# Kernel optimization log

Hardware: AMD Instinct MI355X
Metric: run time of the kernel (lower is better)

The kernel has to match this reference:

```python
import jax, jax.numpy as jnp
import numpy as np

B, S, HID = 4, 2048, 1024
NH, NKV, HD = 16, 4, 64
GROUPS = NH // NKV
SCALE = HD ** -0.5


def make_rope(seq_len, dim, base=10000.0):
    inv_freq = 1.0 / (base ** (np.arange(0, dim, 2, dtype=np.float32) / dim))
    t = np.arange(seq_len, dtype=np.float32)
    freqs = np.outer(t, inv_freq)                      # [S, D/2]
    emb = np.concatenate([freqs, freqs], axis=-1)      # [S, D] duplicated-half convention
    cos = jnp.asarray(np.cos(emb))[None, None]         # [1,1,S,D]
    sin = jnp.asarray(np.sin(emb))[None, None]
    return cos, sin


def setup_inputs() -> dict:
    key = jax.random.key(0)
    ks = jax.random.split(key, 8)
    hidden_states = jax.random.normal(ks[0], (B, S, HID), dtype=jnp.float32)
    cos, sin = make_rope(S, HD)
    std = HID ** -0.5
    Wq = jax.random.normal(ks[1], (NH * HD, HID), dtype=jnp.float32) * std
    bq = jnp.zeros((NH * HD,), dtype=jnp.float32)
    Wk = jax.random.normal(ks[2], (NKV * HD, HID), dtype=jnp.float32) * std
    bk = jnp.zeros((NKV * HD,), dtype=jnp.float32)
    Wv = jax.random.normal(ks[3], (NKV * HD, HID), dtype=jnp.float32) * std
    bv = jnp.zeros((NKV * HD,), dtype=jnp.float32)
    Wo = jax.random.normal(ks[4], (HID, NH * HD), dtype=jnp.float32) * std
    bo = jnp.zeros((HID,), dtype=jnp.float32)
    return dict(hidden_states=hidden_states, cos=cos, sin=sin,
                Wq=Wq, bq=bq, Wk=Wk, bk=bk, Wv=Wv, bv=bv, Wo=Wo, bo=bo)


def rotate_half(x):
    x1, x2 = jnp.split(x, 2, axis=-1)
    return jnp.concatenate([-x2, x1], axis=-1)


def reference(hidden_states, cos, sin, Wq, bq, Wk, bk, Wv, bv, Wo, bo):
    x = hidden_states  # [B,S,HID]
    q = (x @ Wq.T + bq).reshape(B, S, NH, HD).transpose(0, 2, 1, 3)    # [B,NH,S,D]
    k = (x @ Wk.T + bk).reshape(B, S, NKV, HD).transpose(0, 2, 1, 3)   # [B,NKV,S,D]
    v = (x @ Wv.T + bv).reshape(B, S, NKV, HD).transpose(0, 2, 1, 3)
    # RoPE
    q = q * cos + rotate_half(q) * sin
    k = k * cos + rotate_half(k) * sin
    # GQA: repeat_interleave kv heads to match q heads
    k = jnp.repeat(k, GROUPS, axis=1)  # [B,NH,S,D]
    v = jnp.repeat(v, GROUPS, axis=1)
    # scaled dot-product attention (no mask, no dropout at eval)
    scores = jnp.einsum('bhqd,bhkd->bhqk', q, k) * SCALE
    attn = jax.nn.softmax(scores, axis=-1)
    out = jnp.einsum('bhqk,bhkd->bhqd', attn, v)       # [B,NH,S,D]
    out = out.transpose(0, 2, 1, 3).reshape(B, S, NH * HD)
    return out @ Wo.T + bo
```

## Files before the change

### kernel.cpp

```cpp
#include <hip/hip_runtime.h>
#include <stdint.h>

#define S_LEN 2048
#define HIDDEN 1024
#define NHEADS 16
#define NKVH 4
#define HDIM 64

typedef __bf16 bf16x8 __attribute__((ext_vector_type(8)));
typedef __bf16 bf16x4 __attribute__((ext_vector_type(4)));
typedef float f32x4 __attribute__((ext_vector_type(4)));
typedef short s16x4 __attribute__((ext_vector_type(4)));
typedef unsigned short U16;

#define OFF_XB   0u
#define OFF_WQB  8388608u
#define OFF_WKB  9437184u
#define OFF_WVB  9699328u
#define OFF_WOB  9961472u
#define OFF_Q    11010048u
#define OFF_K    19398656u
#define OFF_V    21495808u
#define OFF_AWS  OFF_XB

static __device__ __forceinline__ U16 f2bf(float f){
    unsigned u;
    __builtin_memcpy(&u, &f, 4);
    u += 0x7FFFu + ((u >> 16) & 1u);
    return (U16)(u >> 16);
}
static __device__ __forceinline__ uint32_t pkbf(float lo, float hi){
    uint32_t a, b;
    __builtin_memcpy(&a, &lo, 4); a += 0x7FFFu + ((a >> 16) & 1u);
    __builtin_memcpy(&b, &hi, 4); b += 0x7FFFu + ((b >> 16) & 1u);
    return (a >> 16) | (b & 0xFFFF0000u);
}

typedef __attribute__((address_space(3))) uint32_t lds_u32;
typedef const __attribute__((address_space(1))) uint32_t glb_u32;
static __device__ __forceinline__ void glds16(const U16* g, U16* l){
    __builtin_amdgcn_global_load_lds((glb_u32*)g, (lds_u32*)l, 16, 0, 0);
}

__global__ void conv_kernel(const float* __restrict__ X,  const float* __restrict__ Wq,
                            const float* __restrict__ Wk, const float* __restrict__ Wv,
                            const float* __restrict__ Wo, U16* __restrict__ dst)
{
    size_t i4 = (size_t)blockIdx.x * 256 + threadIdx.x;
    size_t e = i4 * 4;
    const float* s;
    if (e < 8388608u)       s = X  + e;
    else if (e < 9437184u)  s = Wq + (e - 8388608u);
    else if (e < 9699328u)  s = Wk + (e - 9437184u);
    else if (e < 9961472u)  s = Wv + (e - 9699328u);
    else                    s = Wo + (e - 9961472u);
    float4 v = *(const float4*)s;
    uint2 o; o.x = pkbf(v.x, v.y); o.y = pkbf(v.z, v.w);
    *(uint2*)(dst + e) = o;
}

__global__ __launch_bounds__(256, 3)
void qkv_kernel(const U16* __restrict__ Xb,
                const U16* __restrict__ Wqb, const U16* __restrict__ Wkb, const U16* __restrict__ Wvb,
                const float* __restrict__ bq, const float* __restrict__ bk, const float* __restrict__ bv,
                const float* __restrict__ cosT, const float* __restrict__ sinT,
                U16* __restrict__ qws, U16* __restrict__ kws, U16* __restrict__ vtws)
{
    __shared__ __align__(16) U16 Asm[128 * 64];
    __shared__ __align__(16) U16 Bsm[128 * 64];

    const int mblk = blockIdx.x;
    const int nblk = blockIdx.y;
    const int tid  = threadIdx.x;
    const int wave = tid >> 6, lane = tid & 63;
    const int ln = lane & 15, quad = lane >> 4;
    const int wm = wave >> 1, wn = wave & 1;

    const U16* Wp; const float* biasp; int region;
    const int nbase = nblk * 128;
    if (nblk < 8)       { Wp = Wqb + (size_t)nbase * HIDDEN;          biasp = bq + nbase;          region = 0; }
    else if (nblk < 10) { Wp = Wkb + (size_t)(nbase - 1024) * HIDDEN; biasp = bk + (nbase - 1024); region = 1; }
    else                { Wp = Wvb + (size_t)(nbase - 1280) * HIDDEN; biasp = bv + (nbase - 1280); region = 2; }
    const U16* Xp = Xb + (size_t)mblk * 128 * HIDDEN;

    f32x4 acc[4][4];
    #pragma unroll
    for (int i = 0; i < 4; i++)
        #pragma unroll
        for (int j = 0; j < 4; j++) acc[i][j] = (f32x4){0.f, 0.f, 0.f, 0.f};

    const int l8 = lane >> 3;
    const int cg = (lane & 7) ^ l8;
    const int sw = ln & 7;

    for (int k0 = 0; k0 < HIDDEN; k0 += 64) {
        __syncthreads();
        #pragma unroll
        for (int t = 0; t < 4; t++) {
            int rbase = wave * 32 + t * 8;
            glds16(Xp + (size_t)(rbase + l8) * HIDDEN + k0 + cg * 8, &Asm[rbase * 64]);
            glds16(Wp + (size_t)(rbase + l8) * HIDDEN + k0 + cg * 8, &Bsm[rbase * 64]);
        }
        __syncthreads();

        bf16x8 af[4][2], bfr[4][2];
        #pragma unroll
        for (int i = 0; i < 4; i++)
            #pragma unroll
            for (int ks = 0; ks < 2; ks++) {
                af[i][ks]  = *(const bf16x8*)(&Asm[(wm * 64 + i * 16 + ln) * 64 + (((ks * 4 + quad) ^ sw) * 8)]);
                bfr[i][ks] = *(const bf16x8*)(&Bsm[(wn * 64 + i * 16 + ln) * 64 + (((ks * 4 + quad) ^ sw) * 8)]);
            }
        #pragma unroll
        for (int i = 0; i < 4; i++)
            #pragma unroll
            for (int j = 0; j < 4; j++) {
                acc[i][j] = __builtin_amdgcn_mfma_f32_16x16x32_bf16(af[i][0], bfr[j][0], acc[i][j], 0, 0, 0);
                acc[i][j] = __builtin_amdgcn_mfma_f32_16x16x32_bf16(af[i][1], bfr[j][1], acc[i][j], 0, 0, 0);
            }
    }

    float bias[4];
    #pragma unroll
    for (int j = 0; j < 4; j++) bias[j] = biasp[wn * 64 + j * 16 + ln];

    const float QSCALE = 0.125f * 1.44269504089f;

    if (region == 2) {
        #pragma unroll
        for (int i = 0; i < 4; i++) {
            int m0 = mblk * 128 + wm * 64 + i * 16 + quad * 4;
            int b = m0 >> 11;
            int st6 = m0 & (S_LEN - 1);
            int tile = st6 >> 6, soff = st6 & 63;
            #pragma unroll
            for (int j = 0; j < 4; j++) {
                int n2 = nbase - 1280 + wn * 64 + j * 16 + ln;
                int hh = n2 >> 6, d = n2 & 63;
                uint2 w;
                w.x = pkbf(acc[i][j][0] + bias[j], acc[i][j][1] + bias[j]);
                w.y = pkbf(acc[i][j][2] + bias[j], acc[i][j][3] + bias[j]);
                *(uint2*)(vtws + ((((size_t)b * NKVH + hh) * 32 + tile) * 64 + d) * 64 + soff) = w;
            }
        }
    } else {
        #pragma unroll
        for (int i = 0; i < 4; i++) {
            #pragma unroll
            for (int r = 0; r < 4; r++) {
                int m = mblk * 128 + wm * 64 + i * 16 + quad * 4 + r;
                int s = m & (S_LEN - 1), b = m >> 11;
                float vals[4];
                #pragma unroll
                for (int j = 0; j < 4; j++) vals[j] = acc[i][j][r] + bias[j];
                float outv[4];
                #pragma unroll
                for (int j = 0; j < 4; j++) {
                    int d = (wn * 64 + j * 16 + ln) & 63;
                    float c  = cosT[s * HDIM + d];
                    float sn = sinT[s * HDIM + d];
                    float partner = vals[j ^ 2];
                    float rot = (d < 32) ? -partner : partner;
                    outv[j] = vals[j] * c + rot * sn;
                }
                if (region == 0) {
                    #pragma unroll
                    for (int j = 0; j < 4; j++) {
                        int n = nbase + wn * 64 + j * 16 + ln;
                        int hh = n >> 6, d = n & 63;
                        qws[(((size_t)b * NHEADS + hh) * S_LEN + s) * HDIM + d] = f2bf(outv[j] * QSCALE);
                    }
                } else {
                    #pragma unroll
                    for (int j = 0; j < 4; j++) {
                        int n2 = nbase - 1024 + wn * 64 + j * 16 + ln;
                        int hh = n2 >> 6, d = n2 & 63;
                        kws[(((size_t)b * NKVH + hh) * S_LEN + s) * HDIM + d] = f2bf(outv[j]);
                    }
                }
            }
        }
    }
}

__global__ __launch_bounds__(256, 2)
void attn_kernel(const U16* __restrict__ qws, const U16* __restrict__ kws,
                 const U16* __restrict__ vtws, U16* __restrict__ aws)
{
    __shared__ __align__(16) U16 Ksm[2][64 * 64];
    __shared__ __align__(16) U16 VTsm[2][64 * 64];

    const int qt = blockIdx.x;
    const int hg = blockIdx.y;
    const int b = hg >> 4, h = hg & 15, hkv = h >> 2;
    const U16* Qh  = qws  + (size_t)hg * S_LEN * HDIM;
    const U16* Kh  = kws  + (size_t)(b * NKVH + hkv) * S_LEN * HDIM;
    const U16* VTh = vtws + (size_t)(b * NKVH + hkv) * HDIM * S_LEN;

    const int tid = threadIdx.x;
    const int wave = tid >> 6, lane = tid & 63;
    const int ln = lane & 15, quad = lane >> 4;
    const int sw = ln & 7;
    const int off = (quad & 1) * 4;

    bf16x8 qf[2][2];
    #pragma unroll
    for (int i = 0; i < 2; i++)
        #pragma unroll
        for (int ks = 0; ks < 2; ks++) {
            int row = qt * 128 + wave * 32 + i * 16 + ln;
            qf[i][ks] = *(const bf16x8*)(Qh + (size_t)row * HDIM + ks * 32 + quad * 8);
        }

    float rsA[2] = {0.f, 0.f}, rsB[2] = {0.f, 0.f};
    f32x4 o_t[4][2];
    #pragma unroll
    for (int n = 0; n < 4; n++)
        #pragma unroll
        for (int i = 0; i < 2; i++) o_t[n][i] = (f32x4){0.f, 0.f, 0.f, 0.f};

    const int l8 = lane >> 3;
    const int cgk = (lane & 7) ^ l8;

    const U16* pk[2]; const U16* pv[2];
    U16* dK[2]; U16* dV[2];
    #pragma unroll
    for (int t = 0; t < 2; t++) {
        int c = wave * 2 + t;
        pk[t] = Kh  + (size_t)(c * 8 + l8) * HDIM + cgk * 8;
        pv[t] = VTh + (size_t)(c * 8 + l8) * 64  + cgk * 8;
        dK[t] = &Ksm[0][c * 8 * 64];
        dV[t] = &VTsm[0][c * 8 * 64];
    }

    #pragma unroll
    for (int t = 0; t < 2; t++) {
        glds16(pk[t], dK[t]);
        glds16(pv[t], dV[t]);
        pk[t] += 4096; pv[t] += 4096;
    }

    int p = 0;
    for (int kt = 0; kt < 32; kt++) {
        __syncthreads();

        if (kt < 31) {
            #pragma unroll
            for (int t = 0; t < 2; t++) {
                glds16(pk[t], dK[t] + (p ^ 1) * 4096);
                glds16(pv[t], dV[t] + (p ^ 1) * 4096);
                pk[t] += 4096; pv[t] += 4096;
            }
        }

        bf16x8 kf[4][2];
        #pragma unroll
        for (int j4 = 0; j4 < 4; j4++) {
            int row = j4 * 16 + ln;
            kf[j4][0] = *(const bf16x8*)(&Ksm[p][row * 64 + ((quad ^ sw) * 8)]);
            kf[j4][1] = *(const bf16x8*)(&Ksm[p][row * 64 + (((quad + 4) ^ sw) * 8)]);
        }
        s16x4 vf[4][4];
        #pragma unroll
        for (int j4 = 0; j4 < 4; j4++) {
            int cbase = j4 * 2 + (quad >> 1);
            #pragma unroll
            for (int n = 0; n < 4; n++)
                vf[j4][n] = *(const s16x4*)(&VTsm[p][(n * 16 + ln) * 64 + ((cbase ^ sw) * 8) + off]);
        }
        __builtin_amdgcn_sched_barrier(0);

        #pragma unroll
        for (int j4 = 0; j4 < 4; j4++) {
            s16x4 pf[2];
            #pragma unroll
            for (int i = 0; i < 2; i++) {
                f32x4 z = (f32x4){0.f, 0.f, 0.f, 0.f};
                z = __builtin_amdgcn_mfma_f32_16x16x32_bf16(kf[j4][0], qf[i][0], z, 0, 0, 0);
                z = __builtin_amdgcn_mfma_f32_16x16x32_bf16(kf[j4][1], qf[i][1], z, 0, 0, 0);
                bf16x4 pb;
                #pragma unroll
                for (int r = 0; r < 4; r++) {
                    float pv2 = __builtin_amdgcn_exp2f(z[r]);
                    if (r & 1) rsB[i] += pv2; else rsA[i] += pv2;
                    pb[r] = (__bf16)pv2;
                }
                __builtin_memcpy(&pf[i], &pb, 8);
            }
            #pragma unroll
            for (int n = 0; n < 4; n++) {
                #pragma unroll
                for (int i = 0; i < 2; i++)
                    o_t[n][i] = __builtin_amdgcn_mfma_f32_16x16x16bf16_1k(vf[j4][n], pf[i], o_t[n][i], 0, 0, 0);
            }
        }
        p ^= 1;
    }

    float inv_li[2];
    #pragma unroll
    for (int i = 0; i < 2; i++) {
        float t = rsA[i] + rsB[i];
        t += __shfl_xor(t, 16);
        t += __shfl_xor(t, 32);
        inv_li[i] = 1.f / t;
    }
    #pragma unroll
    for (int n = 0; n < 4; n++)
        #pragma unroll
        for (int i = 0; i < 2; i++) {
            int q = qt * 128 + wave * 32 + i * 16 + ln;
            int d = n * 16 + quad * 4;
            uint2 w;
            w.x = pkbf(o_t[n][i][0] * inv_li[i], o_t[n][i][1] * inv_li[i]);
            w.y = pkbf(o_t[n][i][2] * inv_li[i], o_t[n][i][3] * inv_li[i]);
            *(uint2*)(aws + ((size_t)b * S_LEN + q) * (NHEADS * HDIM) + h * HDIM + d) = w;
        }
}

__global__ __launch_bounds__(256, 3)
void proj_kernel(const U16* __restrict__ A, const U16* __restrict__ Wob,
                 const float* __restrict__ bo, float* __restrict__ out)
{
    __shared__ __align__(16) U16 Asm[128 * 64];
    __shared__ __align__(16) U16 Bsm[128 * 64];

    const int mblk = blockIdx.x;
    const int nblk = blockIdx.y;
    const int tid  = threadIdx.x;
    const int wave = tid >> 6, lane = tid & 63;
    const int ln = lane & 15, quad = lane >> 4;
    const int wm = wave >> 1, wn = wave & 1;

    const int nbase = nblk * 128;
    const U16* Wp = Wob + (size_t)nbase * HIDDEN;
    const U16* Ap = A + (size_t)mblk * 128 * HIDDEN;

    f32x4 acc[4][4];
    #pragma unroll
    for (int i = 0; i < 4; i++)
        #pragma unroll
        for (int j = 0; j < 4; j++) acc[i][j] = (f32x4){0.f, 0.f, 0.f, 0.f};

    const int l8 = lane >> 3;
    const int cg = (lane & 7) ^ l8;
    const int sw = ln & 7;

    for (int k0 = 0; k0 < HIDDEN; k0 += 64) {
        __syncthreads();
        #pragma unroll
        for (int t = 0; t < 4; t++) {
            int rbase = wave * 32 + t * 8;
            glds16(Ap + (size_t)(rbase + l8) * HIDDEN + k0 + cg * 8, &Asm[rbase * 64]);
            glds16(Wp + (size_t)(rbase + l8) * HIDDEN + k0 + cg * 8, &Bsm[rbase * 64]);
        }
        __syncthreads();

        bf16x8 af[4][2], bfr[4][2];
        #pragma unroll
        for (int i = 0; i < 4; i++)
            #pragma unroll
            for (int ks = 0; ks < 2; ks++) {
                af[i][ks]  = *(const bf16x8*)(&Asm[(wm * 64 + i * 16 + ln) * 64 + (((ks * 4 + quad) ^ sw) * 8)]);
                bfr[i][ks] = *(const bf16x8*)(&Bsm[(wn * 64 + i * 16 + ln) * 64 + (((ks * 4 + quad) ^ sw) * 8)]);
            }
        #pragma unroll
        for (int i = 0; i < 4; i++)
            #pragma unroll
            for (int j = 0; j < 4; j++) {
                acc[i][j] = __builtin_amdgcn_mfma_f32_16x16x32_bf16(af[i][0], bfr[j][0], acc[i][j], 0, 0, 0);
                acc[i][j] = __builtin_amdgcn_mfma_f32_16x16x32_bf16(af[i][1], bfr[j][1], acc[i][j], 0, 0, 0);
            }
    }

    float bias[4];
    #pragma unroll
    for (int j = 0; j < 4; j++) bias[j] = bo[nbase + wn * 64 + j * 16 + ln];

    #pragma unroll
    for (int i = 0; i < 4; i++)
        #pragma unroll
        for (int r = 0; r < 4; r++) {
            int m = mblk * 128 + wm * 64 + i * 16 + quad * 4 + r;
            #pragma unroll
            for (int j = 0; j < 4; j++) {
                int n = nbase + wn * 64 + j * 16 + ln;
                out[(size_t)m * HIDDEN + n] = acc[i][j][r] + bias[j];
            }
        }
}

extern "C" void kernel_launch(void* const* d_in, const int* in_sizes, int n_in,
                              void* d_out, int out_size, void* d_ws, size_t ws_size,
                              hipStream_t stream)
{
    const float* X    = (const float*)d_in[0];
    const float* cosT = (const float*)d_in[1];
    const float* sinT = (const float*)d_in[2];
    const float* Wq   = (const float*)d_in[3];
    const float* bq   = (const float*)d_in[4];
    const float* Wk   = (const float*)d_in[5];
    const float* bk   = (const float*)d_in[6];
    const float* Wv   = (const float*)d_in[7];
    const float* bv   = (const float*)d_in[8];
    const float* Wo   = (const float*)d_in[9];
    const float* bo   = (const float*)d_in[10];
    float* out = (float*)d_out;

    U16* wsb = (U16*)d_ws;
    U16* Xb   = wsb + OFF_XB;
    U16* Wqb  = wsb + OFF_WQB;
    U16* Wkb  = wsb + OFF_WKB;
    U16* Wvb  = wsb + OFF_WVB;
    U16* Wob  = wsb + OFF_WOB;
    U16* qws  = wsb + OFF_Q;
    U16* kws  = wsb + OFF_K;
    U16* vtws = wsb + OFF_V;
    U16* aws  = wsb + OFF_AWS;

    conv_kernel<<<dim3(10752), 256, 0, stream>>>(X, Wq, Wk, Wv, Wo, wsb);
    qkv_kernel<<<dim3(64, 12), 256, 0, stream>>>(Xb, Wqb, Wkb, Wvb, bq, bk, bv, cosT, sinT, qws, kws, vtws);
    attn_kernel<<<dim3(16, 64), 256, 0, stream>>>(qws, kws, vtws, aws);
    proj_kernel<<<dim3(64, 8), 256, 0, stream>>>(aws, Wob, bo, out);
}
```

Baseline: 255.3 us.

## Software-pipeline attention inner loop, deferring PV MFMA by one step

Restructures the attention key-tile loop so each step issues the QK^T MFMAs for the current 16-key chunk together with the deferred PV MFMAs from the previous chunk. LDS loads for K and V^T are spread across iterations rather than all issued up front. The chunk's exp2 then runs in the shadow of the matrix work, aiming to hide exp and LDS latency behind MFMA. It also raises launch bounds to 4 blocks per CU and uses s_setprio around the MFMA block. The added carried registers and the tighter register budget from the higher occupancy target could cause spills.

After: 244.7 us. 4.2% less time.

```diff
diff --git a/kernel.cpp b/kernel.cpp
--- a/kernel.cpp
+++ b/kernel.cpp
@@ -183,7 +183,7 @@
     }
 }
 
-__global__ __launch_bounds__(256, 2)
+__global__ __launch_bounds__(256, 4)
 void attn_kernel(const U16* __restrict__ qws, const U16* __restrict__ kws,
                  const U16* __restrict__ vtws, U16* __restrict__ aws)
 {
@@ -201,7 +201,7 @@
     const int wave = tid >> 6, lane = tid & 63;
     const int ln = lane & 15, quad = lane >> 4;
     const int sw = ln & 7;
-    const int off = (quad & 1) * 4;
+    const int voff = (quad & 1) * 4;
 
     bf16x8 qf[2][2];
     #pragma unroll
@@ -221,6 +221,13 @@
 
     const int l8 = lane >> 3;
     const int cgk = (lane & 7) ^ l8;
+
+    const int koff0 = ln * 64 + ((quad ^ sw) * 8);
+    const int koff1 = ln * 64 + (((quad + 4) ^ sw) * 8);
+    const int vbase = ln * 64 + voff;
+    int cvo[4];
+    #pragma unroll
+    for (int j = 0; j < 4; j++) cvo[j] = (((j * 2 + (quad >> 1)) ^ sw) * 8);
 
     const U16* pk[2]; const U16* pv[2];
     U16* dK[2]; U16* dV[2];
@@ -240,6 +247,12 @@
         pk[t] += 4096; pv[t] += 4096;
     }
 
+    s16x4 pfp[2];
+    pfp[0] = (s16x4){0, 0, 0, 0}; pfp[1] = (s16x4){0, 0, 0, 0};
+    s16x4 vfp[4];
+    #pragma unroll
+    for (int n = 0; n < 4; n++) vfp[n] = (s16x4){0, 0, 0, 0};
+
     int p = 0;
     for (int kt = 0; kt < 32; kt++) {
         __syncthreads();
@@ -253,49 +266,64 @@
             }
         }
 
-        bf16x8 kf[4][2];
-        #pragma unroll
-        for (int j4 = 0; j4 < 4; j4++) {
-            int row = j4 * 16 + ln;
-            kf[j4][0] = *(const bf16x8*)(&Ksm[p][row * 64 + ((quad ^ sw) * 8)]);
-            kf[j4][1] = *(const bf16x8*)(&Ksm[p][row * 64 + (((quad + 4) ^ sw) * 8)]);
-        }
-        s16x4 vf[4][4];
-        #pragma unroll
-        for (int j4 = 0; j4 < 4; j4++) {
-            int cbase = j4 * 2 + (quad >> 1);
+        const U16* Kb = &Ksm[p][0];
+        const U16* Vb = &VTsm[p][0];
+
+        bf16x8 kfa = *(const bf16x8*)(Kb + koff0);
+        bf16x8 kfb = *(const bf16x8*)(Kb + koff1);
+
+        #pragma unroll
+        for (int j = 0; j < 4; j++) {
+            __builtin_amdgcn_s_setprio(1);
+            f32x4 z[2];
+            #pragma unroll
+            for (int i = 0; i < 2; i++) {
+                z[i] = (f32x4){0.f, 0.f, 0.f, 0.f};
+                z[i] = __builtin_amdgcn_mfma_f32_16x16x32_bf16(kfa, qf[i][0], z[i], 0, 0, 0);
+                z[i] = __builtin_amdgcn_mfma_f32_16x16x32_bf16(kfb, qf[i][1], z[i], 0, 0, 0);
+            }
             #pragma unroll
             for (int n = 0; n < 4; n++)
-                vf[j4][n] = *(const s16x4*)(&VTsm[p][(n * 16 + ln) * 64 + ((cbase ^ sw) * 8) + off]);
-        }
-        __builtin_amdgcn_sched_barrier(0);
-
-        #pragma unroll
-        for (int j4 = 0; j4 < 4; j4++) {
+                #pragma unroll
+                for (int i = 0; i < 2; i++)
+                    o_t[n][i] = __builtin_amdgcn_mfma_f32_16x16x16bf16_1k(vfp[n], pfp[i], o_t[n][i], 0, 0, 0);
+            __builtin_amdgcn_s_setprio(0);
+
+            if (j < 3) {
+                kfa = *(const bf16x8*)(Kb + (j + 1) * 1024 + koff0);
+                kfb = *(const bf16x8*)(Kb + (j + 1) * 1024 + koff1);
+            }
+            s16x4 vf[4];
+            const U16* Vj = Vb + vbase + cvo[j];
+            #pragma unroll
+            for (int n = 0; n < 4; n++)
+                vf[n] = *(const s16x4*)(Vj + n * 1024);
+            __builtin_amdgcn_sched_barrier(0);
+
             s16x4 pf[2];
             #pragma unroll
             for (int i = 0; i < 2; i++) {
-                f32x4 z = (f32x4){0.f, 0.f, 0.f, 0.f};
-                z = __builtin_amdgcn_mfma_f32_16x16x32_bf16(kf[j4][0], qf[i][0], z, 0, 0, 0);
-                z = __builtin_amdgcn_mfma_f32_16x16x32_bf16(kf[j4][1], qf[i][1], z, 0, 0, 0);
                 bf16x4 pb;
                 #pragma unroll
                 for (int r = 0; r < 4; r++) {
-                    float pv2 = __builtin_amdgcn_exp2f(z[r]);
-                    if (r & 1) rsB[i] += pv2; else rsA[i] += pv2;
-                    pb[r] = (__bf16)pv2;
+                    float pe = __builtin_amdgcn_exp2f(z[i][r]);
+                    if (r & 1) rsB[i] += pe; else rsA[i] += pe;
+                    pb[r] = (__bf16)pe;
                 }
                 __builtin_memcpy(&pf[i], &pb, 8);
             }
             #pragma unroll
-            for (int n = 0; n < 4; n++) {
-                #pragma unroll
-                for (int i = 0; i < 2; i++)
-                    o_t[n][i] = __builtin_amdgcn_mfma_f32_16x16x16bf16_1k(vf[j4][n], pf[i], o_t[n][i], 0, 0, 0);
-            }
+            for (int n = 0; n < 4; n++) vfp[n] = vf[n];
+            pfp[0] = pf[0]; pfp[1] = pf[1];
         }
         p ^= 1;
     }
+
+    #pragma unroll
+    for (int n = 0; n < 4; n++)
+        #pragma unroll
+        for (int i = 0; i < 2; i++)
+            o_t[n][i] = __builtin_amdgcn_mfma_f32_16x16x16bf16_1k(vfp[n], pfp[i], o_t[n][i], 0, 0, 0);
 
     float inv_li[2];
     #pragma unroll
```
